# Performance work log

Hardware: AMD Instinct MI355X
Metric: run time of the kernel (lower is better)

Reference implementation:

```python
import jax, jax.numpy as jnp
import numpy as np

N_NODES = 50000
N_EDGES = 800000
FEAT_IN = 128
POS_IN = 16
EDGE_FEAT_IN = 16
H = 64
L = 4


def _lin(k, fan_in, fan_out):
    kw, kb = jax.random.split(k)
    s = 1.0 / np.sqrt(fan_in)
    W = jax.random.uniform(kw, (fan_in, fan_out), minval=-s, maxval=s, dtype=jnp.float32)
    b = jax.random.uniform(kb, (fan_out,), minval=-s, maxval=s, dtype=jnp.float32)
    return W, b


def setup_inputs() -> dict:
    key = jax.random.key(0)
    ks = jax.random.split(key, 32)
    h = jax.random.normal(ks[0], (N_NODES, FEAT_IN), dtype=jnp.float32)
    e = jax.random.normal(ks[1], (N_EDGES, EDGE_FEAT_IN), dtype=jnp.float32)
    p = jax.random.normal(ks[2], (N_NODES, POS_IN), dtype=jnp.float32)
    edge_index = jax.random.randint(ks[3], (2, N_EDGES), 0, N_NODES, dtype=jnp.int64 if jax.config.x64_enabled else jnp.int32)
    he_W, he_b = _lin(ks[4], FEAT_IN, H)
    ee_W, ee_b = _lin(ks[5], EDGE_FEAT_IN, H)
    pe_W, pe_b = _lin(ks[6], POS_IN, H)

    def stack(fan_in, base):
        Ws, bs = [], []
        for i in range(L):
            W, b = _lin(jax.random.fold_in(ks[7], base * 100 + i), fan_in, H)
            Ws.append(W); bs.append(b)
        return jnp.stack(Ws), jnp.stack(bs)

    hm_W, hm_b = stack(5 * H, 0)  # h_message_mlp
    hu_W, hu_b = stack(2 * H, 1)  # h_update
    eu_W, eu_b = stack(3 * H, 2)  # e_update
    pm_W, pm_b = stack(3 * H, 3)  # p_message_mlp
    pu_W, pu_b = stack(2 * H, 4)  # p_update
    return dict(h=h, e=e, p=p, edge_index=edge_index,
                he_W=he_W, he_b=he_b, ee_W=ee_W, ee_b=ee_b, pe_W=pe_W, pe_b=pe_b,
                hm_W=hm_W, hm_b=hm_b, hu_W=hu_W, hu_b=hu_b,
                eu_W=eu_W, eu_b=eu_b, pm_W=pm_W, pm_b=pm_b, pu_W=pu_W, pu_b=pu_b)


def reference(h, e, p, edge_index, he_W, he_b, ee_W, ee_b, pe_W, pe_b,
              hm_W, hm_b, hu_W, hu_b, eu_W, eu_b, pm_W, pm_b, pu_W, pu_b):
    send, rec = edge_index[0], edge_index[1]
    n = h.shape[0]
    h = h @ he_W + he_b  # [N,H]
    e = e @ ee_W + ee_b  # [E,H]
    p = p @ pe_W + pe_b  # [N,H]
    for i in range(L):
        hp_send = jnp.concatenate((h[send], p[send]), axis=1)  # [E,2H]
        hp_rec = jnp.concatenate((h[rec], p[rec]), axis=1)     # [E,2H]
        h_msg = jnp.concatenate((hp_send, hp_rec, e), axis=1) @ hm_W[i] + hm_b[i]  # [E,H]
        h_agg = jax.ops.segment_sum(h_msg, rec, num_segments=n)  # [N,H]
        h = jnp.concatenate((h, h_agg), axis=1) @ hu_W[i] + hu_b[i]
        e = jnp.concatenate((h[send], h[rec], e), axis=1) @ eu_W[i] + eu_b[i]
        p_msg = jnp.concatenate((p[send], p[rec], e), axis=1) @ pm_W[i] + pm_b[i]
        p_agg = jax.ops.segment_sum(p_msg, rec, num_segments=n)
        p = jnp.concatenate((p, p_agg), axis=1) @ pu_W[i] + pu_b[i]
    return (h, p)
```

## Files before the change

kernel.cpp:

```cpp
#include <hip/hip_runtime.h>
#include <hip/hip_bf16.h>

#define NN 50000
#define NE 800000

typedef __hip_bfloat16 bf16;
typedef __attribute__((ext_vector_type(8))) short bf16x8s;
typedef __attribute__((ext_vector_type(4))) float f32x4;

#define OFF_HP     0L
#define OFF_HSUM   12800000L
#define OFF_PSUM   25600000L
#define OFF_ESUM   38400000L
#define OFF_EAGGA  41600000L
#define OFF_EAGGB  54400000L
#define OFF_WFMT   67200000L
#define OFF_ROWPTR 67716096L
#define OFF_COLIDX 67916100L
#define OFF_SSEND  71116100L
#define OFF_SEG    74316100L
#define OFF_CNT    77516100L
#define OFF_BSUM   77716100L

#define SCAN_B 196

#define FW_HE 0
#define FW_EE 8192
#define FW_PE 10240
#define FW_L0 12288
#define LSTR  61440
#define R_HAGG 0
#define R_HMR  12288
#define R_HU   20480
#define R_EUS  28672
#define R_EUR  32768
#define R_EUE  36864
#define R_PAGG 40960
#define R_PMR  49152
#define R_PU   53248

#define AGG_STRIDE 72

__device__ __forceinline__ bf16x8s bfrag(const bf16* w, int c, int t, int lane) {
    return *(const bf16x8s*)(w + ((long)(c*4 + t)*64 + lane)*8);
}
__device__ __forceinline__ bf16x8s cvt8(const float* fp) {
    float4 f0 = ((const float4*)fp)[0];
    float4 f1 = ((const float4*)fp)[1];
    bf16 tmp[8];
    tmp[0]=__float2bfloat16(f0.x); tmp[1]=__float2bfloat16(f0.y);
    tmp[2]=__float2bfloat16(f0.z); tmp[3]=__float2bfloat16(f0.w);
    tmp[4]=__float2bfloat16(f1.x); tmp[5]=__float2bfloat16(f1.y);
    tmp[6]=__float2bfloat16(f1.z); tmp[7]=__float2bfloat16(f1.w);
    return *(const bf16x8s*)tmp;
}

__global__ __launch_bounds__(256) void wfmt_k(
    const float* __restrict__ he, const float* __restrict__ ee, const float* __restrict__ pe,
    const float* __restrict__ hm, const float* __restrict__ hu, const float* __restrict__ eu,
    const float* __restrict__ pm, const float* __restrict__ pu, bf16* __restrict__ wf)
{
    int s = blockIdx.x;
    const float* src = nullptr; int rowoff = 0, Ksrc = 0, Kpad = 0, mode = 0, split = 0, gap = 0; long doff = 0;
    if      (s == 0) { src = he; Ksrc = 128; Kpad = 128; doff = FW_HE; }
    else if (s == 1) { src = ee; Ksrc = 16;  Kpad = 32;  doff = FW_EE; }
    else if (s == 2) { src = pe; Ksrc = 16;  Kpad = 32;  doff = FW_PE; }
    else {
        int i = (s - 3) / 9, g = (s - 3) % 9;
        long base = FW_L0 + (long)i*LSTR;
        const float* HM = hm + (long)i*320*64;
        const float* HU = hu + (long)i*128*64;
        const float* EU = eu + (long)i*192*64;
        const float* PM = pm + (long)i*192*64;
        const float* PU = pu + (long)i*128*64;
        switch (g) {
          case 0:  src=HM; mode=4; split=128; gap=128; Kpad=192; doff=base+R_HAGG; break;
          case 1:  src=HM; rowoff=128; Ksrc=128; Kpad=128; doff=base+R_HMR;  break;
          case 2:  src=HU; rowoff=0;   Ksrc=128; Kpad=128; doff=base+R_HU;   break;
          case 3:  src=EU; rowoff=0;   Ksrc=64;  Kpad=64;  doff=base+R_EUS;  break;
          case 4:  src=EU; rowoff=64;  Ksrc=64;  Kpad=64;  doff=base+R_EUR;  break;
          case 5:  src=EU; rowoff=128; Ksrc=64;  Kpad=64;  doff=base+R_EUE;  break;
          case 6:  src=PM; mode=4; split=64; gap=64; Kpad=128; doff=base+R_PAGG; break;
          case 7:  src=PM; rowoff=64;  Ksrc=64;  Kpad=64;  doff=base+R_PMR;  break;
          default: src=PU; rowoff=0;   Ksrc=128; Kpad=128; doff=base+R_PU;   break;
        }
    }
    int total = Kpad * 64;
    for (int idx = threadIdx.x; idx < total; idx += 256) {
        int j = idx & 7, l = (idx >> 3) & 63, ct = idx >> 9;
        int c = ct >> 2, t = ct & 3;
        int k = c*32 + (l >> 4)*8 + j;
        int n = t*16 + (l & 15);
        float v;
        if (mode == 4) v = src[(long)(k + (k >= split ? gap : 0))*64 + n];
        else           v = (k < Ksrc) ? src[(long)(rowoff + k)*64 + n] : 0.f;
        wf[doff + idx] = __float2bfloat16(v);
    }
}

__global__ __launch_bounds__(256) void hist_k(const int* __restrict__ rec, int* __restrict__ cnt)
{
    int e = blockIdx.x*256 + threadIdx.x;
    if (e < NE) atomicAdd(&cnt[rec[e]], 1);
}

__global__ __launch_bounds__(256) void scan1_k(const int* __restrict__ cnt, int* __restrict__ bsum)
{
    __shared__ int sdata[256];
    int tid = threadIdx.x;
    int i = blockIdx.x*256 + tid;
    sdata[tid] = (i < NN) ? cnt[i] : 0;
    __syncthreads();
    #pragma unroll
    for (int off = 128; off > 0; off >>= 1) {
        if (tid < off) sdata[tid] += sdata[tid + off];
        __syncthreads();
    }
    if (tid == 0) bsum[blockIdx.x] = sdata[0];
}

__global__ __launch_bounds__(256) void scan2_k(int* __restrict__ bsum)
{
    __shared__ int sdata[256];
    int tid = threadIdx.x;
    int v = (tid < SCAN_B) ? bsum[tid] : 0;
    sdata[tid] = v;
    __syncthreads();
    #pragma unroll
    for (int off = 1; off < 256; off <<= 1) {
        int t = (tid >= off) ? sdata[tid - off] : 0;
        __syncthreads();
        sdata[tid] += t;
        __syncthreads();
    }
    if (tid < SCAN_B) bsum[tid] = sdata[tid] - v;
}

__global__ __launch_bounds__(256) void scan3_k(const int* __restrict__ cnt,
    const int* __restrict__ bsum, int* __restrict__ rowptr)
{
    __shared__ int sdata[256];
    int tid = threadIdx.x;
    int i = blockIdx.x*256 + tid;
    sdata[tid] = (i < NN) ? cnt[i] : 0;
    __syncthreads();
    #pragma unroll
    for (int off = 1; off < 256; off <<= 1) {
        int t = (tid >= off) ? sdata[tid - off] : 0;
        __syncthreads();
        sdata[tid] += t;
        __syncthreads();
    }
    if (i < NN) rowptr[i + 1] = sdata[tid] + bsum[blockIdx.x];
    if (i == 0) rowptr[0] = 0;
}

__global__ __launch_bounds__(256) void scatter_k(const int* __restrict__ rec,
    const int* __restrict__ rowptr, int* __restrict__ cursor, int* __restrict__ colidx)
{
    int e = blockIdx.x*256 + threadIdx.x;
    if (e < NE) {
        int r = rec[e];
        int pos = atomicAdd(&cursor[r], 1);
        __builtin_nontemporal_store(e, &colidx[rowptr[r] + pos]);
    }
}

__global__ __launch_bounds__(256) void segfill_k(const int* __restrict__ rowptr, int* __restrict__ seg)
{
    int n = blockIdx.x*256 + threadIdx.x;
    if (n < NN) {
        int b = rowptr[n], e = rowptr[n + 1];
        for (int j = b; j < e; ++j) seg[j] = n;
    }
}

__global__ __launch_bounds__(256) void gsum64_k(const bf16* __restrict__ hp, int coff,
    const int* __restrict__ ssend, const int* __restrict__ seg, float* __restrict__ out)
{
    __shared__ int s_ids[256];
    __shared__ int s_seg[256];
    int tid = threadIdx.x, lane = tid & 63, wv = tid >> 6;
    int gbase = blockIdx.x*256;
    s_ids[tid] = ssend[gbase + tid];
    s_seg[tid] = seg[gbase + tid];
    __syncthreads();
    int j0 = wv*64;
    const bf16* base = hp + coff + lane;

    unsigned short va[16], vb[16];
    #pragma unroll
    for (int k = 0; k < 16; ++k)
        va[k] = *(const unsigned short*)(base + (long)s_ids[j0 + k]*128);

    float a = 0.f;
    int cur = s_seg[j0];
    #pragma unroll
    for (int b = 0; b < 4; ++b) {
        if (b < 3) {
            #pragma unroll
            for (int k = 0; k < 16; ++k)
                vb[k] = *(const unsigned short*)(base + (long)s_ids[j0 + (b+1)*16 + k]*128);
        }
        #pragma unroll
        for (int k = 0; k < 16; ++k) {
            int n = s_seg[j0 + b*16 + k];
            if (n != cur) { atomicAdd(&out[(long)cur*64 + lane], a); a = 0.f; cur = n; }
            a += __uint_as_float(((unsigned)va[k]) << 16);
        }
        if (b < 3) {
            #pragma unroll
            for (int k = 0; k < 16; ++k) va[k] = vb[k];
        }
    }
    atomicAdd(&out[(long)cur*64 + lane], a);
}

__global__ __launch_bounds__(256) void esum_k(const float* __restrict__ e_in,
    const int* __restrict__ colidx, const int* __restrict__ seg, const int* __restrict__ send,
    int* __restrict__ ssend, float* __restrict__ esum)
{
    __shared__ int s_ids[256];
    __shared__ int s_seg[256];
    int tid = threadIdx.x;
    int gbase = blockIdx.x*256;
    int id = colidx[gbase + tid];
    s_ids[tid] = id;
    s_seg[tid] = seg[gbase + tid];
    ssend[gbase + tid] = send[id];
    __syncthreads();
    int grp = tid >> 4, c = tid & 15;
    int j0 = grp*16;
    float vv[16];
    #pragma unroll
    for (int jj = 0; jj < 16; ++jj) vv[jj] = e_in[(long)s_ids[j0 + jj]*16 + c];
    float a = 0.f;
    int cur = s_seg[j0];
    #pragma unroll
    for (int jj = 0; jj < 16; ++jj) {
        int n = s_seg[j0 + jj];
        if (n != cur) { atomicAdd(&esum[(long)cur*16 + c], a); a = 0.f; cur = n; }
        a += vv[jj];
    }
    atomicAdd(&esum[(long)cur*16 + c], a);
}

__global__ __launch_bounds__(256) void eembn_k(const float* __restrict__ esum,
    const int* __restrict__ deg, const bf16* __restrict__ wEE, const float* __restrict__ ee_b,
    float* __restrict__ eagg)
{
    int tid = threadIdx.x, lane = tid & 63, wv = tid >> 6;
    int l15 = lane & 15, q = lane >> 4;
    int row = blockIdx.x*64 + wv*16 + l15;
    int rc = (row < NN) ? row : NN - 1;
    f32x4 acc[4];
    #pragma unroll
    for (int t = 0; t < 4; ++t) { acc[t][0]=0; acc[t][1]=0; acc[t][2]=0; acc[t][3]=0; }
    {
        bf16x8s af = {0,0,0,0,0,0,0,0};
        if (q < 2) af = cvt8(esum + (long)rc*16 + q*8);
        #pragma unroll
        for (int t = 0; t < 4; ++t)
            acc[t] = __builtin_amdgcn_mfma_f32_16x16x32_bf16(af, bfrag(wEE, 0, t, lane), acc[t], 0, 0, 0);
    }
    float bv[4];
    #pragma unroll
    for (int t = 0; t < 4; ++t) bv[t] = ee_b[t*16 + l15];
    #pragma unroll
    for (int r = 0; r < 4; ++r) {
        int ro = blockIdx.x*64 + wv*16 + q*4 + r;
        if (ro < NN) {
            float dg = (float)deg[ro];
            #pragma unroll
            for (int t = 0; t < 4; ++t)
                eagg[(long)ro*64 + t*16 + l15] = acc[t][r] + dg*bv[t];
        }
    }
}

__global__ __launch_bounds__(256) void hemb_k(const float* __restrict__ h_in,
    const bf16* __restrict__ wHE, const float* __restrict__ he_b, bf16* __restrict__ hp)
{
    int tid = threadIdx.x, lane = tid & 63, wv = tid >> 6;
    int l15 = lane & 15, q = lane >> 4;
    int row = blockIdx.x*64 + wv*16 + l15;
    int rc = (row < NN) ? row : NN - 1;
    f32x4 acc[4];
    #pragma unroll
    for (int t = 0; t < 4; ++t) { float b = he_b[t*16 + l15]; acc[t][0]=b; acc[t][1]=b; acc[t][2]=b; acc[t][3]=b; }
    #pragma unroll
    for (int c = 0; c < 4; ++c) {
        bf16x8s af = cvt8(h_in + (long)rc*128 + c*32 + q*8);
        #pragma unroll
        for (int t = 0; t < 4; ++t)
            acc[t] = __builtin_amdgcn_mfma_f32_16x16x32_bf16(af, bfrag(wHE, c, t, lane), acc[t], 0, 0, 0);
    }
    #pragma unroll
    for (int r = 0; r < 4; ++r) {
        int ro = blockIdx.x*64 + wv*16 + q*4 + r;
        if (ro < NN)
            #pragma unroll
            for (int t = 0; t < 4; ++t) hp[(long)ro*128 + t*16 + l15] = __float2bfloat16(acc[t][r]);
    }
}

__global__ __launch_bounds__(256) void pemb_k(const float* __restrict__ p_in,
    const bf16* __restrict__ wPE, const float* __restrict__ pe_b, bf16* __restrict__ hp)
{
    int tid = threadIdx.x, lane = tid & 63, wv = tid >> 6;
    int l15 = lane & 15, q = lane >> 4;
    int row = blockIdx.x*64 + wv*16 + l15;
    int rc = (row < NN) ? row : NN - 1;
    f32x4 acc[4];
    #pragma unroll
    for (int t = 0; t < 4; ++t) { float b = pe_b[t*16 + l15]; acc[t][0]=b; acc[t][1]=b; acc[t][2]=b; acc[t][3]=b; }
    {
        bf16x8s af = {0,0,0,0,0,0,0,0};
        if (q < 2) af = cvt8(p_in + (long)rc*16 + q*8);
        #pragma unroll
        for (int t = 0; t < 4; ++t)
            acc[t] = __builtin_amdgcn_mfma_f32_16x16x32_bf16(af, bfrag(wPE, 0, t, lane), acc[t], 0, 0, 0);
    }
    #pragma unroll
    for (int r = 0; r < 4; ++r) {
        int ro = blockIdx.x*64 + wv*16 + q*4 + r;
        if (ro < NN)
            #pragma unroll
            for (int t = 0; t < 4; ++t) hp[(long)ro*128 + 64 + t*16 + l15] = __float2bfloat16(acc[t][r]);
    }
}

__global__ __launch_bounds__(256) void hfuse_k(
    bf16* __restrict__ hp, float* __restrict__ hsum, const float* __restrict__ psum,
    const float* __restrict__ eagg, const int* __restrict__ deg,
    const bf16* __restrict__ wAGG, const bf16* __restrict__ wR, const float* __restrict__ mb,
    const bf16* __restrict__ wU, const float* __restrict__ ub, float* __restrict__ out2)
{
    __shared__ __align__(16) bf16 sAgg[64 * AGG_STRIDE];
    int tid = threadIdx.x, lane = tid & 63, wv = tid >> 6;
    int l15 = lane & 15, q = lane >> 4;
    int row = blockIdx.x*64 + wv*16 + l15;
    int rc = (row < NN) ? row : NN - 1;

    f32x4 aA[4], aR[4];
    #pragma unroll
    for (int t = 0; t < 4; ++t) {
        aA[t][0]=0;aA[t][1]=0;aA[t][2]=0;aA[t][3]=0;
        aR[t][0]=0;aR[t][1]=0;aR[t][2]=0;aR[t][3]=0;
    }
    #pragma unroll
    for (int c = 0; c < 6; ++c) {
        bf16x8s af = (c < 2) ? cvt8(hsum + (long)rc*64 + c*32 + q*8)
                   : (c < 4) ? cvt8(psum + (long)rc*64 + (c-2)*32 + q*8)
                             : cvt8(eagg + (long)rc*64 + (c-4)*32 + q*8);
        #pragma unroll
        for (int t = 0; t < 4; ++t)
            aA[t] = __builtin_amdgcn_mfma_f32_16x16x32_bf16(af, bfrag(wAGG, c, t, lane), aA[t], 0, 0, 0);
    }
    if (row < NN) {
        float4 z4 = make_float4(0.f, 0.f, 0.f, 0.f);
        #pragma unroll
        for (int c = 0; c < 2; ++c) {
            *(float4*)(hsum + (long)rc*64 + c*32 + q*8)     = z4;
            *(float4*)(hsum + (long)rc*64 + c*32 + q*8 + 4) = z4;
        }
    }
    #pragma unroll
    for (int c = 0; c < 4; ++c) {
        bf16x8s af = *(const bf16x8s*)(hp + (long)rc*128 + c*32 + q*8);
        #pragma unroll
        for (int t = 0; t < 4; ++t)
            aR[t] = __builtin_amdgcn_mfma_f32_16x16x32_bf16(af, bfrag(wR, c, t, lane), aR[t], 0, 0, 0);
    }
    float mbv[4];
    #pragma unroll
    for (int t = 0; t < 4; ++t) mbv[t] = mb[t*16 + l15];
    #pragma unroll
    for (int r = 0; r < 4; ++r) {
        int ro = blockIdx.x*64 + wv*16 + q*4 + r;
        float dg = (float)deg[(ro < NN) ? ro : NN - 1];
        #pragma unroll
        for (int t = 0; t < 4; ++t)
            sAgg[(wv*16 + q*4 + r)*AGG_STRIDE + t*16 + l15] =
                __float2bfloat16(aA[t][r] + dg*(aR[t][r] + mbv[t]));
    }
    __syncthreads();
    f32x4 acc[4];
    #pragma unroll
    for (int t = 0; t < 4; ++t) { float b = ub[t*16 + l15]; acc[t][0]=b; acc[t][1]=b; acc[t][2]=b; acc[t][3]=b; }
    #pragma unroll
    for (int c = 0; c < 4; ++c) {
        bf16x8s af = (c < 2) ? *(const bf16x8s*)(hp + (long)rc*128 + c*32 + q*8)
                             : *(const bf16x8s*)(sAgg + (wv*16 + l15)*AGG_STRIDE + (c-2)*32 + q*8);
        #pragma unroll
        for (int t = 0; t < 4; ++t)
            acc[t] = __builtin_amdgcn_mfma_f32_16x16x32_bf16(af, bfrag(wU, c, t, lane), acc[t], 0, 0, 0);
    }
    #pragma unroll
    for (int r = 0; r < 4; ++r) {
        int ro = blockIdx.x*64 + wv*16 + q*4 + r;
        if (ro < NN) {
            #pragma unroll
            for (int t = 0; t < 4; ++t) {
                float fv = acc[t][r];
                hp[(long)ro*128 + t*16 + l15] = __float2bfloat16(fv);
                if (out2) out2[(long)ro*64 + t*16 + l15] = fv;
            }
        }
    }
}

__global__ __launch_bounds__(256) void pfuse_k(
    bf16* __restrict__ hp, const float* __restrict__ hsumN, float* __restrict__ psum,
    const float* __restrict__ eaggIn, float* __restrict__ eaggOut, const int* __restrict__ deg,
    const bf16* __restrict__ wEUS, const bf16* __restrict__ wEUR, const bf16* __restrict__ wEUE,
    const float* __restrict__ eub,
    const bf16* __restrict__ wAGG, const bf16* __restrict__ wR, const float* __restrict__ mb,
    const bf16* __restrict__ wU, const float* __restrict__ ub, float* __restrict__ out2)
{
    __shared__ __align__(16) bf16 sE[64 * AGG_STRIDE];
    __shared__ __align__(16) bf16 sAgg[64 * AGG_STRIDE];
    int tid = threadIdx.x, lane = tid & 63, wv = tid >> 6;
    int l15 = lane & 15, q = lane >> 4;
    int row = blockIdx.x*64 + wv*16 + l15;
    int rc = (row < NN) ? row : NN - 1;

    f32x4 aE[4], aH[4];
    #pragma unroll
    for (int t = 0; t < 4; ++t) {
        aE[t][0]=0;aE[t][1]=0;aE[t][2]=0;aE[t][3]=0;
        aH[t][0]=0;aH[t][1]=0;aH[t][2]=0;aH[t][3]=0;
    }
    #pragma unroll
    for (int c = 0; c < 4; ++c) {
        bf16x8s af = (c < 2) ? cvt8(hsumN + (long)rc*64 + c*32 + q*8)
                             : cvt8(eaggIn + (long)rc*64 + (c-2)*32 + q*8);
        #pragma unroll
        for (int t = 0; t < 4; ++t) {
            bf16x8s w = (c < 2) ? bfrag(wEUS, c, t, lane) : bfrag(wEUE, c-2, t, lane);
            aE[t] = __builtin_amdgcn_mfma_f32_16x16x32_bf16(af, w, aE[t], 0, 0, 0);
        }
    }
    #pragma unroll
    for (int c = 0; c < 2; ++c) {
        bf16x8s af = *(const bf16x8s*)(hp + (long)rc*128 + c*32 + q*8);
        #pragma unroll
        for (int t = 0; t < 4; ++t)
            aH[t] = __builtin_amdgcn_mfma_f32_16x16x32_bf16(af, bfrag(wEUR, c, t, lane), aH[t], 0, 0, 0);
    }
    float ebv[4];
    #pragma unroll
    for (int t = 0; t < 4; ++t) ebv[t] = eub[t*16 + l15];
    #pragma unroll
    for (int r = 0; r < 4; ++r) {
        int ro = blockIdx.x*64 + wv*16 + q*4 + r;
        float dg = (float)deg[(ro < NN) ? ro : NN - 1];
        #pragma unroll
        for (int t = 0; t < 4; ++t) {
            float ev = aE[t][r] + dg*(aH[t][r] + ebv[t]);
            sE[(wv*16 + q*4 + r)*AGG_STRIDE + t*16 + l15] = __float2bfloat16(ev);
            if (ro < NN) eaggOut[(long)ro*64 + t*16 + l15] = ev;
        }
    }
    __syncthreads();

    f32x4 aA[4], aR[4];
    #pragma unroll
    for (int t = 0; t < 4; ++t) {
        aA[t][0]=0;aA[t][1]=0;aA[t][2]=0;aA[t][3]=0;
        aR[t][0]=0;aR[t][1]=0;aR[t][2]=0;aR[t][3]=0;
    }
    #pragma unroll
    for (int c = 0; c < 4; ++c) {
        bf16x8s af = (c < 2) ? cvt8(psum + (long)rc*64 + c*32 + q*8)
                             : *(const bf16x8s*)(sE + (wv*16 + l15)*AGG_STRIDE + (c-2)*32 + q*8);
        #pragma unroll
        for (int t = 0; t < 4; ++t)
            aA[t] = __builtin_amdgcn_mfma_f32_16x16x32_bf16(af, bfrag(wAGG, c, t, lane), aA[t], 0, 0, 0);
    }
    if (row < NN) {
        float4 z4 = make_float4(0.f, 0.f, 0.f, 0.f);
        #pragma unroll
        for (int c = 0; c < 2; ++c) {
            *(float4*)(psum + (long)rc*64 + c*32 + q*8)     = z4;
            *(float4*)(psum + (long)rc*64 + c*32 + q*8 + 4) = z4;
        }
    }
    #pragma unroll
    for (int c = 0; c < 2; ++c) {
        bf16x8s af = *(const bf16x8s*)(hp + (long)rc*128 + 64 + c*32 + q*8);
        #pragma unroll
        for (int t = 0; t < 4; ++t)
            aR[t] = __builtin_amdgcn_mfma_f32_16x16x32_bf16(af, bfrag(wR, c, t, lane), aR[t], 0, 0, 0);
    }
    float mbv[4];
    #pragma unroll
    for (int t = 0; t < 4; ++t) mbv[t] = mb[t*16 + l15];
    #pragma unroll
    for (int r = 0; r < 4; ++r) {
        int ro = blockIdx.x*64 + wv*16 + q*4 + r;
        float dg = (float)deg[(ro < NN) ? ro : NN - 1];
        #pragma unroll
        for (int t = 0; t < 4; ++t)
            sAgg[(wv*16 + q*4 + r)*AGG_STRIDE + t*16 + l15] =
                __float2bfloat16(aA[t][r] + dg*(aR[t][r] + mbv[t]));
    }
    __syncthreads();
    f32x4 acc[4];
    #pragma unroll
    for (int t = 0; t < 4; ++t) { float b = ub[t*16 + l15]; acc[t][0]=b; acc[t][1]=b; acc[t][2]=b; acc[t][3]=b; }
    #pragma unroll
    for (int c = 0; c < 4; ++c) {
        bf16x8s af = (c < 2) ? *(const bf16x8s*)(hp + (long)rc*128 + 64 + c*32 + q*8)
                             : *(const bf16x8s*)(sAgg + (wv*16 + l15)*AGG_STRIDE + (c-2)*32 + q*8);
        #pragma unroll
        for (int t = 0; t < 4; ++t)
            acc[t] = __builtin_amdgcn_mfma_f32_16x16x32_bf16(af, bfrag(wU, c, t, lane), acc[t], 0, 0, 0);
    }
    #pragma unroll
    for (int r = 0; r < 4; ++r) {
        int ro = blockIdx.x*64 + wv*16 + q*4 + r;
        if (ro < NN) {
            #pragma unroll
            for (int t = 0; t < 4; ++t) {
                float fv = acc[t][r];
                hp[(long)ro*128 + 64 + t*16 + l15] = __float2bfloat16(fv);
                if (out2) out2[(long)ro*64 + t*16 + l15] = fv;
            }
        }
    }
}

extern "C" void kernel_launch(void* const* d_in, const int* in_sizes, int n_in,
                              void* d_out, int out_size, void* d_ws, size_t ws_size,
                              hipStream_t stream)
{
    (void)in_sizes; (void)n_in; (void)out_size; (void)ws_size;
    const float* h_in = (const float*)d_in[0];
    const float* e_in = (const float*)d_in[1];
    const float* p_in = (const float*)d_in[2];
    const int*  ei   = (const int*)d_in[3];
    const int* send = ei;
    const int* rec  = ei + NE;
    const float* he_W = (const float*)d_in[4];  const float* he_b = (const float*)d_in[5];
    const float* ee_W = (const float*)d_in[6];  const float* ee_b = (const float*)d_in[7];
    const float* pe_W = (const float*)d_in[8];  const float* pe_b = (const float*)d_in[9];
    const float* hm_W = (const float*)d_in[10]; const float* hm_b = (const float*)d_in[11];
    const float* hu_W = (const float*)d_in[12]; const float* hu_b = (const float*)d_in[13];
    const float* eu_W = (const float*)d_in[14]; const float* eu_b = (const float*)d_in[15];
    const float* pm_W = (const float*)d_in[16]; const float* pm_b = (const float*)d_in[17];
    const float* pu_W = (const float*)d_in[18]; const float* pu_b = (const float*)d_in[19];

    char* ws = (char*)d_ws;
    bf16* hp     = (bf16*)(ws + OFF_HP);
    float* hsum  = (float*)(ws + OFF_HSUM);
    float* psum  = (float*)(ws + OFF_PSUM);
    float* esum  = (float*)(ws + OFF_ESUM);
    float* eaggA = (float*)(ws + OFF_EAGGA);
    float* eaggB = (float*)(ws + OFF_EAGGB);
    bf16* wf     = (bf16*)(ws + OFF_WFMT);
    int* rowptr  = (int*)(ws + OFF_ROWPTR);
    int* colidx  = (int*)(ws + OFF_COLIDX);
    int* ssend   = (int*)(ws + OFF_SSEND);
    int* segarr  = (int*)(ws + OFF_SEG);
    int* cnt     = (int*)(ws + OFF_CNT);
    int* bsum    = (int*)(ws + OFF_BSUM);
    float* dout  = (float*)d_out;

    const int EB   = NE / 256;
    const int NB64 = (NN + 63) / 64;

    (void)hipMemsetAsync(cnt, 0, NN * sizeof(int), stream);
    hist_k<<<EB, 256, 0, stream>>>(rec, cnt);
    scan1_k<<<SCAN_B, 256, 0, stream>>>(cnt, bsum);
    scan2_k<<<1, 256, 0, stream>>>(bsum);
    scan3_k<<<SCAN_B, 256, 0, stream>>>(cnt, bsum, rowptr);
    (void)hipMemsetAsync(cnt, 0, NN * sizeof(int), stream);
    scatter_k<<<EB, 256, 0, stream>>>(rec, rowptr, cnt, colidx);
    segfill_k<<<SCAN_B, 256, 0, stream>>>(rowptr, segarr);

    (void)hipMemsetAsync(hsum, 0, (long)NN*(64 + 64 + 16)*sizeof(float), stream);

    esum_k<<<EB, 256, 0, stream>>>(e_in, colidx, segarr, send, ssend, esum);

    wfmt_k<<<39, 256, 0, stream>>>(he_W, ee_W, pe_W, hm_W, hu_W, eu_W, pm_W, pu_W, wf);

    hemb_k<<<NB64, 256, 0, stream>>>(h_in, wf + FW_HE, he_b, hp);
    pemb_k<<<NB64, 256, 0, stream>>>(p_in, wf + FW_PE, pe_b, hp);
    eembn_k<<<NB64, 256, 0, stream>>>(esum, cnt, wf + FW_EE, ee_b, eaggA);
    gsum64_k<<<EB, 256, 0, stream>>>(hp, 0,  ssend, segarr, hsum);
    gsum64_k<<<EB, 256, 0, stream>>>(hp, 64, ssend, segarr, psum);

    float* eA = eaggA;
    float* eB = eaggB;
    for (int i = 0; i < 4; ++i) {
        long base = FW_L0 + (long)i*LSTR;
        hfuse_k<<<NB64, 256, 0, stream>>>(hp, hsum, psum, eA, cnt,
            wf + base + R_HAGG, wf + base + R_HMR, hm_b + i*64,
            wf + base + R_HU, hu_b + i*64,
            (i == 3) ? dout : nullptr);
        gsum64_k<<<EB, 256, 0, stream>>>(hp, 0, ssend, segarr, hsum);
        pfuse_k<<<NB64, 256, 0, stream>>>(hp, hsum, psum, eA, eB, cnt,
            wf + base + R_EUS, wf + base + R_EUR, wf + base + R_EUE, eu_b + i*64,
            wf + base + R_PAGG, wf + base + R_PMR, pm_b + i*64,
            wf + base + R_PU, pu_b + i*64,
            (i == 3) ? dout + (long)NN*64 : nullptr);
        if (i < 3)
            gsum64_k<<<EB, 256, 0, stream>>>(hp, 64, ssend, segarr, psum);
        float* tmp = eA; eA = eB; eB = tmp;
    }
}
```

Before: 645.6 us.

## Replace atomic edge-parallel segment sums with node-parallel CSR gather-sums

```diff
diff --git a/kernel.cpp b/kernel.cpp
--- a/kernel.cpp
+++ b/kernel.cpp
@@ -18,7 +18,6 @@
 #define OFF_ROWPTR 67716096L
 #define OFF_COLIDX 67916100L
 #define OFF_SSEND  71116100L
-#define OFF_SEG    74316100L
 #define OFF_CNT    77516100L
 #define OFF_BSUM   77716100L
 
@@ -166,83 +165,91 @@
     }
 }
 
-__global__ __launch_bounds__(256) void segfill_k(const int* __restrict__ rowptr, int* __restrict__ seg)
-{
-    int n = blockIdx.x*256 + threadIdx.x;
-    if (n < NN) {
-        int b = rowptr[n], e = rowptr[n + 1];
-        for (int j = b; j < e; ++j) seg[j] = n;
-    }
-}
-
-__global__ __launch_bounds__(256) void gsum64_k(const bf16* __restrict__ hp, int coff,
-    const int* __restrict__ ssend, const int* __restrict__ seg, float* __restrict__ out)
-{
-    __shared__ int s_ids[256];
-    __shared__ int s_seg[256];
-    int tid = threadIdx.x, lane = tid & 63, wv = tid >> 6;
-    int gbase = blockIdx.x*256;
-    s_ids[tid] = ssend[gbase + tid];
-    s_seg[tid] = seg[gbase + tid];
-    __syncthreads();
-    int j0 = wv*64;
-    const bf16* base = hp + coff + lane;
-
-    unsigned short va[16], vb[16];
-    #pragma unroll
-    for (int k = 0; k < 16; ++k)
-        va[k] = *(const unsigned short*)(base + (long)s_ids[j0 + k]*128);
-
-    float a = 0.f;
-    int cur = s_seg[j0];
-    #pragma unroll
-    for (int b = 0; b < 4; ++b) {
-        if (b < 3) {
-            #pragma unroll
-            for (int k = 0; k < 16; ++k)
-                vb[k] = *(const unsigned short*)(base + (long)s_ids[j0 + (b+1)*16 + k]*128);
-        }
+__global__ __launch_bounds__(256) void ssend_k(const int* __restrict__ colidx,
+    const int* __restrict__ send, int* __restrict__ ssend)
+{
+    int j = blockIdx.x*256 + threadIdx.x;
+    if (j < NE) ssend[j] = send[colidx[j]];
+}
+
+template <bool BOTH>
+__global__ __launch_bounds__(256) void gsumn_k(const bf16* __restrict__ hp, int coff,
+    const int* __restrict__ rowptr, const int* __restrict__ ssend,
+    float* __restrict__ out1, float* __restrict__ out2)
+{
+    int tid = threadIdx.x, lane = tid & 63, wv = tid >> 6;
+    int nb = blockIdx.x*64 + wv*16;
+    if (nb >= NN) return;
+    int ne = nb + 16; if (ne > NN) ne = NN;
+    int jb = rowptr[nb], je = rowptr[ne];
+
+    unsigned short va[16], vb[16], wa[16], wb[16];
+    int m0 = je - jb; if (m0 > 16) m0 = 16;
+    #pragma unroll
+    for (int k = 0; k < 16; ++k) {
+        if (k < m0) {
+            long o = (long)ssend[jb + k]*128 + coff + lane;
+            va[k] = *(const unsigned short*)(hp + o);
+            if (BOTH) wa[k] = *(const unsigned short*)(hp + o + 64);
+        }
+    }
+    float a = 0.f, b = 0.f;
+    int n = nb, nend = rowptr[n + 1];
+    for (int j = jb; j < je; j += 16) {
+        int mn = je - (j + 16); mn = mn < 0 ? 0 : (mn > 16 ? 16 : mn);
         #pragma unroll
         for (int k = 0; k < 16; ++k) {
-            int n = s_seg[j0 + b*16 + k];
-            if (n != cur) { atomicAdd(&out[(long)cur*64 + lane], a); a = 0.f; cur = n; }
-            a += __uint_as_float(((unsigned)va[k]) << 16);
-        }
-        if (b < 3) {
-            #pragma unroll
-            for (int k = 0; k < 16; ++k) va[k] = vb[k];
-        }
-    }
-    atomicAdd(&out[(long)cur*64 + lane], a);
-}
-
-__global__ __launch_bounds__(256) void esum_k(const float* __restrict__ e_in,
-    const int* __restrict__ colidx, const int* __restrict__ seg, const int* __restrict__ send,
-    int* __restrict__ ssend, float* __restrict__ esum)
-{
-    __shared__ int s_ids[256];
-    __shared__ int s_seg[256];
-    int tid = threadIdx.x;
-    int gbase = blockIdx.x*256;
-    int id = colidx[gbase + tid];
-    s_ids[tid] = id;
-    s_seg[tid] = seg[gbase + tid];
-    ssend[gbase + tid] = send[id];
-    __syncthreads();
-    int grp = tid >> 4, c = tid & 15;
-    int j0 = grp*16;
-    float vv[16];
-    #pragma unroll
-    for (int jj = 0; jj < 16; ++jj) vv[jj] = e_in[(long)s_ids[j0 + jj]*16 + c];
-    float a = 0.f;
-    int cur = s_seg[j0];
-    #pragma unroll
-    for (int jj = 0; jj < 16; ++jj) {
-        int n = s_seg[j0 + jj];
-        if (n != cur) { atomicAdd(&esum[(long)cur*16 + c], a); a = 0.f; cur = n; }
-        a += vv[jj];
-    }
-    atomicAdd(&esum[(long)cur*16 + c], a);
+            if (k < mn) {
+                long o = (long)ssend[j + 16 + k]*128 + coff + lane;
+                vb[k] = *(const unsigned short*)(hp + o);
+                if (BOTH) wb[k] = *(const unsigned short*)(hp + o + 64);
+            }
+        }
+        int m = je - j; if (m > 16) m = 16;
+        #pragma unroll
+        for (int k = 0; k < 16; ++k) {
+            if (k < m) {
+                int jj = j + k;
+                while (jj >= nend) {
+                    out1[(long)n*64 + lane] = a;
+                    if (BOTH) out2[(long)n*64 + lane] = b;
+                    a = 0.f; b = 0.f;
+                    ++n; nend = rowptr[n + 1];
+                }
+                a += __uint_as_float(((unsigned)va[k]) << 16);
+                if (BOTH) b += __uint_as_float(((unsigned)wa[k]) << 16);
+            }
+        }
+        #pragma unroll
+        for (int k = 0; k < 16; ++k) { va[k] = vb[k]; if (BOTH) wa[k] = wb[k]; }
+    }
+    while (n < ne) {
+        out1[(long)n*64 + lane] = a;
+        if (BOTH) out2[(long)n*64 + lane] = b;
+        a = 0.f; b = 0.f;
+        ++n;
+    }
+}
+
+__global__ __launch_bounds__(256) void esumn_k(const float* __restrict__ e_in,
+    const int* __restrict__ rowptr, const int* __restrict__ colidx,
+    float* __restrict__ esum)
+{
+    int tid = threadIdx.x, lane = tid & 63, wv = tid >> 6;
+    int g = lane >> 4, c = lane & 15;
+    int nb = blockIdx.x*64 + wv*16;
+    if (nb >= NN) return;
+    #pragma unroll
+    for (int t = 0; t < 4; ++t) {
+        int n = nb + g*4 + t;
+        if (n < NN) {
+            float a = 0.f;
+            int b = rowptr[n], e = rowptr[n + 1];
+            for (int j = b; j < e; ++j)
+                a += e_in[(long)colidx[j]*16 + c];
+            esum[(long)n*16 + c] = a;
+        }
+    }
 }
 
 __global__ __launch_bounds__(256) void eembn_k(const float* __restrict__ esum,
@@ -331,7 +338,7 @@
 }
 
 __global__ __launch_bounds__(256) void hfuse_k(
-    bf16* __restrict__ hp, float* __restrict__ hsum, const float* __restrict__ psum,
+    bf16* __restrict__ hp, const float* __restrict__ hsum, const float* __restrict__ psum,
     const float* __restrict__ eagg, const int* __restrict__ deg,
     const bf16* __restrict__ wAGG, const bf16* __restrict__ wR, const float* __restrict__ mb,
     const bf16* __restrict__ wU, const float* __restrict__ ub, float* __restrict__ out2)
@@ -356,14 +363,6 @@
         #pragma unroll
         for (int t = 0; t < 4; ++t)
             aA[t] = __builtin_amdgcn_mfma_f32_16x16x32_bf16(af, bfrag(wAGG, c, t, lane), aA[t], 0, 0, 0);
-    }
-    if (row < NN) {
-        float4 z4 = make_float4(0.f, 0.f, 0.f, 0.f);
-        #pragma unroll
-        for (int c = 0; c < 2; ++c) {
-            *(float4*)(hsum + (long)rc*64 + c*32 + q*8)     = z4;
-            *(float4*)(hsum + (long)rc*64 + c*32 + q*8 + 4) = z4;
-        }
     }
     #pragma unroll
     for (int c = 0; c < 4; ++c) {
@@ -411,7 +410,7 @@
 }
 
 __global__ __launch_bounds__(256) void pfuse_k(
-    bf16* __restrict__ hp, const float* __restrict__ hsumN, float* __restrict__ psum,
+    bf16* __restrict__ hp, const float* __restrict__ hsumN, const float* __restrict__ psum,
     const float* __restrict__ eaggIn, float* __restrict__ eaggOut, const int* __restrict__ deg,
     const bf16* __restrict__ wEUS, const bf16* __restrict__ wEUR, const bf16* __restrict__ wEUE,
     const float* __restrict__ eub,
@@ -459,7 +458,7 @@
         for (int t = 0; t < 4; ++t) {
             float ev = aE[t][r] + dg*(aH[t][r] + ebv[t]);
             sE[(wv*16 + q*4 + r)*AGG_STRIDE + t*16 + l15] = __float2bfloat16(ev);
-            if (ro < NN) eaggOut[(long)ro*64 + t*16 + l15] = ev;
+            if (eaggOut && ro < NN) eaggOut[(long)ro*64 + t*16 + l15] = ev;
         }
     }
     __syncthreads();
@@ -477,14 +476,6 @@
         #pragma unroll
         for (int t = 0; t < 4; ++t)
             aA[t] = __builtin_amdgcn_mfma_f32_16x16x32_bf16(af, bfrag(wAGG, c, t, lane), aA[t], 0, 0, 0);
-    }
-    if (row < NN) {
-        float4 z4 = make_float4(0.f, 0.f, 0.f, 0.f);
-        #pragma unroll
-        for (int c = 0; c < 2; ++c) {
-            *(float4*)(psum + (long)rc*64 + c*32 + q*8)     = z4;
-            *(float4*)(psum + (long)rc*64 + c*32 + q*8 + 4) = z4;
-        }
     }
     #pragma unroll
     for (int c = 0; c < 2; ++c) {
@@ -562,7 +553,6 @@
     int* rowptr  = (int*)(ws + OFF_ROWPTR);
     int* colidx  = (int*)(ws + OFF_COLIDX);
     int* ssend   = (int*)(ws + OFF_SSEND);
-    int* segarr  = (int*)(ws + OFF_SEG);
     int* cnt     = (int*)(ws + OFF_CNT);
     int* bsum    = (int*)(ws + OFF_BSUM);
     float* dout  = (float*)d_out;
@@ -577,19 +567,15 @@
     scan3_k<<<SCAN_B, 256, 0, stream>>>(cnt, bsum, rowptr);
     (void)hipMemsetAsync(cnt, 0, NN * sizeof(int), stream);
     scatter_k<<<EB, 256, 0, stream>>>(rec, rowptr, cnt, colidx);
-    segfill_k<<<SCAN_B, 256, 0, stream>>>(rowptr, segarr);
-
-    (void)hipMemsetAsync(hsum, 0, (long)NN*(64 + 64 + 16)*sizeof(float), stream);
-
-    esum_k<<<EB, 256, 0, stream>>>(e_in, colidx, segarr, send, ssend, esum);
+    ssend_k<<<EB, 256, 0, stream>>>(colidx, send, ssend);
 
     wfmt_k<<<39, 256, 0, stream>>>(he_W, ee_W, pe_W, hm_W, hu_W, eu_W, pm_W, pu_W, wf);
 
+    esumn_k<<<NB64, 256, 0, stream>>>(e_in, rowptr, colidx, esum);
     hemb_k<<<NB64, 256, 0, stream>>>(h_in, wf + FW_HE, he_b, hp);
     pemb_k<<<NB64, 256, 0, stream>>>(p_in, wf + FW_PE, pe_b, hp);
     eembn_k<<<NB64, 256, 0, stream>>>(esum, cnt, wf + FW_EE, ee_b, eaggA);
-    gsum64_k<<<EB, 256, 0, stream>>>(hp, 0,  ssend, segarr, hsum);
-    gsum64_k<<<EB, 256, 0, stream>>>(hp, 64, ssend, segarr, psum);
+    gsumn_k<true><<<NB64, 256, 0, stream>>>(hp, 0, rowptr, ssend, hsum, psum);
 
     float* eA = eaggA;
     float* eB = eaggB;
@@ -599,14 +585,14 @@
             wf + base + R_HAGG, wf + base + R_HMR, hm_b + i*64,
             wf + base + R_HU, hu_b + i*64,
             (i == 3) ? dout : nullptr);
-        gsum64_k<<<EB, 256, 0, stream>>>(hp, 0, ssend, segarr, hsum);
-        pfuse_k<<<NB64, 256, 0, stream>>>(hp, hsum, psum, eA, eB, cnt,
+        gsumn_k<false><<<NB64, 256, 0, stream>>>(hp, 0, rowptr, ssend, hsum, nullptr);
+        pfuse_k<<<NB64, 256, 0, stream>>>(hp, hsum, psum, eA, (i < 3) ? eB : nullptr, cnt,
             wf + base + R_EUS, wf + base + R_EUR, wf + base + R_EUE, eu_b + i*64,
             wf + base + R_PAGG, wf + base + R_PMR, pm_b + i*64,
             wf + base + R_PU, pu_b + i*64,
             (i == 3) ? dout + (long)NN*64 : nullptr);
         if (i < 3)
-            gsum64_k<<<EB, 256, 0, stream>>>(hp, 64, ssend, segarr, psum);
+            gsumn_k<false><<<NB64, 256, 0, stream>>>(hp, 64, rowptr, ssend, psum, nullptr);
         float* tmp = eA; eA = eB; eB = tmp;
     }
 }
```

After: 1.803 ms. 2.79x slower.
